# Optimization experiments

Measured on AMD Instinct MI355X. Metric: run time of the kernel, lower is better.

## Reference

```python
import jax, jax.numpy as jnp
import numpy as np

B, S, D, H = 2, 2048, 1024, 16
DK = D // H
NEG = -1.0e9


def setup_inputs() -> dict:
    key = jax.random.key(0)
    ks = jax.random.split(key, 11)
    inp = {
        "q": jax.random.normal(ks[0], (B, S, D), jnp.float32),
        "k": jax.random.normal(ks[1], (B, S, D), jnp.float32),
        "v": jax.random.normal(ks[2], (B, S, D), jnp.float32),
        "mask": jnp.tril(jnp.ones((S, S), jnp.int32))[None, None],  # causal [1,1,S,S]
    }
    scale = 0.02
    inp["w_q"] = jax.random.normal(ks[3], (D, D), jnp.float32) * scale
    inp["b_q"] = jnp.zeros((D,), jnp.float32)
    inp["w_k"] = jax.random.normal(ks[4], (D, D), jnp.float32) * scale
    inp["b_k"] = jnp.zeros((D,), jnp.float32)
    inp["w_v"] = jax.random.normal(ks[5], (D, D), jnp.float32) * scale
    inp["b_v"] = jnp.zeros((D,), jnp.float32)
    inp["w_o"] = jax.random.normal(ks[6], (D, D), jnp.float32) * scale
    inp["b_o"] = jnp.zeros((D,), jnp.float32)
    return inp


def reference(q, k, v, mask, w_q, b_q, w_k, b_k, w_v, b_v, w_o, b_o):
    # projections: [B,S,D] -> [B,H,S,DK]
    def proj(x, w, b):
        y = jnp.einsum("bsd,de->bse", x, w) + b
        return y.reshape(B, S, H, DK).transpose(0, 2, 1, 3)

    Q = proj(q, w_q, b_q)
    K = proj(k, w_k, b_k)
    V = proj(v, w_v, b_v)
    # explicit scores matrix, faithful to the original naive attention
    scores = jnp.einsum("bhsd,bhtd->bhst", Q, K) / jnp.sqrt(jnp.float32(DK))
    scores = jnp.where(mask == 0, NEG, scores)
    attn = jax.nn.softmax(scores, axis=-1)  # dropout p=0.0 -> identity
    x = jnp.einsum("bhst,bhtd->bhsd", attn, V)
    x = x.transpose(0, 2, 1, 3).reshape(B, S, D)
    return jnp.einsum("bsd,de->bse", x, w_o) + b_o
```

## Files before the change

### kernel.cpp

```cpp
#include <hip/hip_runtime.h>
#include <hip/hip_bf16.h>

typedef __bf16 bf16;
typedef __bf16 bf16x2 __attribute__((ext_vector_type(2)));
typedef __bf16 bf16x8 __attribute__((ext_vector_type(8)));
typedef float f32x4 __attribute__((ext_vector_type(4)));
typedef float f32x16 __attribute__((ext_vector_type(16)));

#define MFMA16(a, b, c) __builtin_amdgcn_mfma_f32_16x16x32_bf16(a, b, c, 0, 0, 0)
#define MFMA32(a, b, c) __builtin_amdgcn_mfma_f32_32x32x16_bf16(a, b, c, 0, 0, 0)

#define QSCALE 0.18033688f

__device__ __forceinline__ void gld16(const bf16* g, bf16* l) {
  __builtin_amdgcn_global_load_lds(
      (const __attribute__((address_space(1))) void*)g,
      (__attribute__((address_space(3))) void*)l, 16, 0, 0);
}

__global__ __launch_bounds__(256) void prep_k(
    const float* __restrict__ w0, const float* __restrict__ w1,
    const float* __restrict__ w2, const float* __restrict__ w3,
    bf16* __restrict__ dst, const float* __restrict__ q,
    const float* __restrict__ k, const float* __restrict__ v,
    bf16* __restrict__ qb, bf16* __restrict__ kb, bf16* __restrict__ vb) {
  const int t = threadIdx.x;
  if (blockIdx.z >= 4) {
    const int zi = blockIdx.z - 4;
    const float* src = zi == 0 ? q : zi == 1 ? k : v;
    bf16* d = zi == 0 ? qb : zi == 1 ? kb : vb;
    const int fb = blockIdx.y * 16 + blockIdx.x;
#pragma unroll
    for (int j = 0; j < 8; ++j) {
      const size_t i = ((size_t)j * 65536 + fb * 256 + t) * 8;
      float4 a = *(const float4*)(src + i);
      float4 b = *(const float4*)(src + i + 4);
      bf16x8 o;
      o[0] = (bf16)a.x; o[1] = (bf16)a.y; o[2] = (bf16)a.z; o[3] = (bf16)a.w;
      o[4] = (bf16)b.x; o[5] = (bf16)b.y; o[6] = (bf16)b.z; o[7] = (bf16)b.w;
      *(bf16x8*)(d + i) = o;
    }
    return;
  }

  __shared__ bf16 T[64][68];
  const float* W = blockIdx.z == 0 ? w0 : blockIdx.z == 1 ? w1
                   : blockIdx.z == 2 ? w2 : w3;
  bf16* Y = dst + (size_t)blockIdx.z * 1024 * 1024;
  const int r = t >> 2, c4 = t & 3;
  const int k0 = blockIdx.y * 64, n0 = blockIdx.x * 64;

  const float4* src = (const float4*)(W + (size_t)(k0 + r) * 1024 + n0 + c4 * 16);
  float4 f0 = src[0], f1 = src[1], f2 = src[2], f3 = src[3];
  bf16* row = &T[r][c4 * 16];
  row[0] = (bf16)f0.x; row[1] = (bf16)f0.y; row[2] = (bf16)f0.z; row[3] = (bf16)f0.w;
  row[4] = (bf16)f1.x; row[5] = (bf16)f1.y; row[6] = (bf16)f1.z; row[7] = (bf16)f1.w;
  row[8] = (bf16)f2.x; row[9] = (bf16)f2.y; row[10] = (bf16)f2.z; row[11] = (bf16)f2.w;
  row[12] = (bf16)f3.x; row[13] = (bf16)f3.y; row[14] = (bf16)f3.z; row[15] = (bf16)f3.w;
  __syncthreads();

  bf16x8 o0, o1;
#pragma unroll
  for (int j = 0; j < 8; ++j) o0[j] = T[c4 * 16 + j][r];
#pragma unroll
  for (int j = 0; j < 8; ++j) o1[j] = T[c4 * 16 + 8 + j][r];
  bf16* d = Y + (size_t)(n0 + r) * 1024 + k0 + c4 * 16;
  *(bf16x8*)d = o0;
  *(bf16x8*)(d + 8) = o1;
}

template <int QKV, int MT>
__global__ __launch_bounds__(256, 3) void gemm_p(
    const bf16* __restrict__ xq, const bf16* __restrict__ xk,
    const bf16* __restrict__ xv, const bf16* __restrict__ Wt,
    const float* __restrict__ bq, const float* __restrict__ bk,
    const float* __restrict__ bv, bf16* __restrict__ Qp,
    bf16* __restrict__ Kp, bf16* __restrict__ Vtp, float* __restrict__ Yf) {
  constexpr int AROWS = MT * 32;
  __shared__ __align__(16) bf16 SH[AROWS * 64 + 128 * 64];
  bf16* Al = SH;
  bf16* Bl = SH + AROWS * 64;

  const int z = QKV ? blockIdx.z : 0;
  const bf16* X = QKV ? (z == 0 ? xq : z == 1 ? xk : xv) : xq;
  const bf16* Bt = Wt + (size_t)z * 1048576;
  const float* bias = QKV ? (z == 0 ? bq : z == 1 ? bk : bv) : bq;
  const float escale = (QKV && z == 0) ? QSCALE : 1.0f;

  const int t = threadIdx.x;
  const int wave = t >> 6, lane = t & 63, quad = lane >> 4, l16 = lane & 15;
  const int wm = (wave >> 1) * (MT * 16), wn = (wave & 1) * 64;
  const int bm = blockIdx.y * AROWS, bn = blockIdx.x * 128;

  const int lr = (lane >> 3) & 7, lc = lane & 7;
  constexpr int NAC = AROWS / 32;
  const bf16* gA[NAC];
  bf16* lA[NAC];
#pragma unroll
  for (int i = 0; i < NAC; ++i) {
    const int q = wave * NAC + i;
    gA[i] = X + (size_t)(bm + 8 * q + lr) * 1024 + 8 * (lc ^ lr);
    lA[i] = Al + q * 512;
  }
  const bf16* gB[4];
  bf16* lB[4];
#pragma unroll
  for (int i = 0; i < 4; ++i) {
    const int q = wave * 4 + i;
    gB[i] = Bt + (size_t)(bn + 8 * q + lr) * 1024 + 8 * (lc ^ lr);
    lB[i] = Bl + q * 512;
  }

  f32x4 acc[MT][4] = {};
  const int fswz = (l16 & 7) << 4;

  for (int kb = 0; kb < 1024; kb += 64) {
    __syncthreads();
#pragma unroll
    for (int i = 0; i < NAC; ++i) gld16(gA[i] + kb, lA[i]);
#pragma unroll
    for (int i = 0; i < 4; ++i) gld16(gB[i] + kb, lB[i]);
    __syncthreads();

#pragma unroll
    for (int kk = 0; kk < 2; ++kk) {
      const int cb = (kk * 64 + quad * 16) ^ fswz;
      bf16x8 af[MT], bfr[4];
#pragma unroll
      for (int mt = 0; mt < MT; ++mt)
        af[mt] = *(const bf16x8*)((const char*)Al +
                                  (wm + mt * 16 + l16) * 128 + cb);
#pragma unroll
      for (int nt = 0; nt < 4; ++nt)
        bfr[nt] = *(const bf16x8*)((const char*)Bl +
                                   (wn + nt * 16 + l16) * 128 + cb);
#pragma unroll
      for (int mt = 0; mt < MT; ++mt)
#pragma unroll
        for (int nt = 0; nt < 4; ++nt)
          acc[mt][nt] = MFMA16(af[mt], bfr[nt], acc[mt][nt]);
    }
  }

  if (QKV && z == 2) {
    bf16* Tt = SH;
    const int b = bm >> 11;
    __syncthreads();
#pragma unroll
    for (int half = 0; half < 2; ++half) {
      if ((wave & 1) == half) {
#pragma unroll
        for (int nt = 0; nt < 4; ++nt) {
          const int ln = nt * 16 + l16;
          const float bia = bias[bn + half * 64 + ln];
#pragma unroll
          for (int mt = 0; mt < 4; ++mt)
#pragma unroll
            for (int r = 0; r < 4; ++r) {
              const int m = wm + mt * 16 + quad * 4 + r;
              Tt[ln * 136 + m] = (bf16)(acc[mt][nt][r] + bia);
            }
        }
      }
      __syncthreads();
      {
        const int ln = t >> 2, seg = (t & 3) * 32;
        const int gn = bn + half * 64 + ln;
        const int h = gn >> 6, dk = gn & 63;
        const int s0 = (bm & 2047) + seg;
        bf16* dstp = Vtp + ((size_t)(b * 16 + h) * 64 + dk) * 2048 + s0;
        const bf16* srcp = Tt + ln * 136 + seg;
#pragma unroll
        for (int j = 0; j < 4; ++j)
          *(bf16x8*)(dstp + j * 8) = *(const bf16x8*)(srcp + j * 8);
      }
      __syncthreads();
    }
  } else {
#pragma unroll
    for (int mt = 0; mt < MT; ++mt)
#pragma unroll
      for (int nt = 0; nt < 4; ++nt) {
        const int gn = bn + wn + nt * 16 + l16;
        const float bia = bias[gn];
#pragma unroll
        for (int r = 0; r < 4; ++r) {
          const int gm = bm + wm + mt * 16 + quad * 4 + r;
          const float val = (acc[mt][nt][r] + bia) * escale;
          if (!QKV) {
            Yf[(size_t)gm * 1024 + gn] = val;
          } else {
            const int b = gm >> 11, s = gm & 2047;
            const int h = gn >> 6, dk = gn & 63;
            bf16* Y = (z == 0) ? Qp : Kp;
            Y[((size_t)(b * 16 + h) * 2048 + s) * 64 + dk] = (bf16)val;
          }
        }
      }
  }
}

__global__ __launch_bounds__(256, 2) void attn_k(const bf16* __restrict__ Q,
                                                 const bf16* __restrict__ K,
                                                 const bf16* __restrict__ Vt,
                                                 bf16* __restrict__ X) {
  __shared__ __align__(16) char LB[65536];
  __shared__ float Ex[2048];
  __shared__ float ExR[128];
  __shared__ float rsL[4][32];

  bf16* KB = (bf16*)LB;
  bf16* VB = (bf16*)(LB + 32768);

  const int t = threadIdx.x;
  const int wave = t >> 6, lane = t & 63;
  const int cl = lane & 31, h = lane >> 5;
  const int qsub = wave & 1, kpart = wave >> 1;

  const int n = blockIdx.x;
  const int xcd = n & 7, mm = n >> 3;
  const int bh = xcd + 8 * (mm & 3);
  const int pairx = mm >> 2;
  const int b = bh >> 4, hh = bh & 15;

  const bf16* Qb = Q + (size_t)bh * 2048 * 64;
  const bf16* Kb = K + (size_t)bh * 2048 * 64;
  const bf16* Vb = Vt + (size_t)bh * 64 * 2048;

  const int lr = (lane >> 3) & 7, lc = lane & 7;
  const int sp = wave & 1;
  const bool isV = wave >= 2;
  const bf16* gsb = isV ? (Vb + (size_t)lr * 2048 + 8 * (lc ^ lr))
                        : (Kb + (size_t)lr * 64 + 8 * (lc ^ lr));
  const size_t cqStep = isV ? 16384 : 512;
  const size_t ktStep = isV ? 64 : 4096;
  bf16* lbs = (isV ? VB : KB) + sp * 4096;

  const int fswz = (cl & 7) << 4;

  for (int ph = 0; ph < 2; ++ph) {
    const int qt = ph ? 31 - pairx : pairx;
    const int ntiles = qt + 1;
    const int S = (ntiles + 1) >> 1;
    const int q0 = qt * 64 + qsub * 32;

    bf16x8 qf[4];
#pragma unroll
    for (int ks = 0; ks < 4; ++ks)
      qf[ks] = *(const bf16x8*)(Qb + (size_t)(q0 + cl) * 64 + ks * 16 + h * 8);

    f32x16 o0 = {}, o1 = {};
    float rs = 0.f;

#pragma unroll
    for (int cq = 0; cq < 8; ++cq)
      gld16(gsb + (size_t)sp * ktStep + cq * cqStep, lbs + cq * 512);
    __syncthreads();

    for (int ss = 0; ss < S; ++ss) {
      const int par = ss & 1;
      const bool more = (ss + 1) < S;
      if (more) {
        const size_t kt2 = 2 * (ss + 1) + sp;
#pragma unroll
        for (int cq = 0; cq < 8; ++cq)
          gld16(gsb + kt2 * ktStep + cq * cqStep,
                lbs + (par ^ 1) * 8192 + cq * 512);
      }

      const int kt = 2 * ss + kpart;
      if (kt < ntiles) {
        const int k0 = kt * 64;
        const char* Kc = (const char*)(KB + (par * 2 + kpart) * 4096);
        const char* Vc = (const char*)(VB + (par * 2 + kpart) * 4096);
        const bool interior = (k0 + 63) <= q0;

        f32x16 s0v = {}, s1v = {};
#pragma unroll
        for (int ks = 0; ks < 4; ++ks) {
          const int cb = ks * 32 + h * 16;
          bf16x8 f0 = *(const bf16x8*)(Kc + cl * 128 + (cb ^ fswz));
          bf16x8 f1 = *(const bf16x8*)(Kc + (cl + 32) * 128 + (cb ^ fswz));
          s0v = MFMA32(f0, qf[ks], s0v);
          s1v = MFMA32(f1, qf[ks], s1v);
        }

        unsigned pk[8][2];
        float ts = 0.f;
        auto smax = [&](const f32x16& sv, int mk) {
#pragma unroll
          for (int sl = 0; sl < 4; ++sl)
#pragma unroll
            for (int p = 0; p < 2; ++p) {
              float e0 = exp2f(sv[sl * 4 + 2 * p]);
              float e1 = exp2f(sv[sl * 4 + 2 * p + 1]);
              if (!interior) {
                const int ky = k0 + mk * 32 + 8 * sl + 4 * h + 2 * p;
                const int qg = q0 + cl;
                if (ky > qg) e0 = 0.f;
                if (ky + 1 > qg) e1 = 0.f;
              }
              ts += e0 + e1;
              union { bf16x2 v; unsigned u; } cv;
              cv.v[0] = (bf16)e0;
              cv.v[1] = (bf16)e1;
              pk[mk * 4 + sl][p] = cv.u;
            }
        };
        smax(s0v, 0);
        smax(s1v, 1);
        rs += ts;

        bf16x8 pf[4];
#pragma unroll
        for (int ks = 0; ks < 4; ++ks) {
          const unsigned oe0 = pk[2 * ks][0], oe1 = pk[2 * ks][1];
          const unsigned oo0 = pk[2 * ks + 1][0], oo1 = pk[2 * ks + 1][1];
          const unsigned pe0 = (unsigned)__shfl_xor((int)oe0, 32, 64);
          const unsigned pe1 = (unsigned)__shfl_xor((int)oe1, 32, 64);
          const unsigned po0 = (unsigned)__shfl_xor((int)oo0, 32, 64);
          const unsigned po1 = (unsigned)__shfl_xor((int)oo1, 32, 64);
          union { unsigned u[4]; bf16x8 v; } fu;
          fu.u[0] = h ? po0 : oe0;
          fu.u[1] = h ? po1 : oe1;
          fu.u[2] = h ? oo0 : pe0;
          fu.u[3] = h ? oo1 : pe1;
          pf[ks] = fu.v;
        }

#pragma unroll
        for (int ks = 0; ks < 4; ++ks) {
          const int cb = ks * 32 + h * 16;
          bf16x8 v0f = *(const bf16x8*)(Vc + cl * 128 + (cb ^ fswz));
          bf16x8 v1f = *(const bf16x8*)(Vc + (cl + 32) * 128 + (cb ^ fswz));
          o0 = MFMA32(pf[ks], v0f, o0);
          o1 = MFMA32(pf[ks], v1f, o1);
        }
      }

      __syncthreads();
    }

    if (kpart == 0) {
      float* e = Ex + qsub * 1024;
#pragma unroll
      for (int i = 0; i < 16; ++i) e[i * 64 + lane] = o0[i];
      ExR[qsub * 64 + lane] = rs;
    }
    __syncthreads();
    if (kpart == 1) {
      const float* e = Ex + qsub * 1024;
#pragma unroll
      for (int i = 0; i < 16; ++i) o0[i] += e[i * 64 + lane];
      rs += ExR[qsub * 64 + lane];
    }
    __syncthreads();
    if (kpart == 0) {
      float* e = Ex + qsub * 1024;
#pragma unroll
      for (int i = 0; i < 16; ++i) e[i * 64 + lane] = o1[i];
    }
    __syncthreads();
    if (kpart == 1) {
      const float* e = Ex + qsub * 1024;
#pragma unroll
      for (int i = 0; i < 16; ++i) o1[i] += e[i * 64 + lane];

      const float rtot = rs + __shfl_xor(rs, 32, 64);
      rsL[wave][cl] = 1.0f / rtot;
      __builtin_amdgcn_s_waitcnt(0xC07F);
      bf16* Xb = X + (size_t)b * 2048 * 1024 + hh * 64;
#pragma unroll
      for (int g = 0; g < 16; ++g) {
        const int qr = (g & 3) + 8 * (g >> 2) + 4 * h;
        const float ri = rsL[wave][qr];
        const int qg = q0 + qr;
        Xb[(size_t)qg * 1024 + cl] = (bf16)(o0[g] * ri);
        Xb[(size_t)qg * 1024 + 32 + cl] = (bf16)(o1[g] * ri);
      }
    }
    __syncthreads();
  }
}

extern "C" void kernel_launch(void* const* d_in, const int* in_sizes, int n_in,
                              void* d_out, int out_size, void* d_ws,
                              size_t ws_size, hipStream_t stream) {
  const float* q = (const float*)d_in[0];
  const float* k = (const float*)d_in[1];
  const float* v = (const float*)d_in[2];
  const float* w_q = (const float*)d_in[4];
  const float* b_q = (const float*)d_in[5];
  const float* w_k = (const float*)d_in[6];
  const float* b_k = (const float*)d_in[7];
  const float* w_v = (const float*)d_in[8];
  const float* b_v = (const float*)d_in[9];
  const float* w_o = (const float*)d_in[10];
  const float* b_o = (const float*)d_in[11];

  bf16* ws = (bf16*)d_ws;
  const size_t NELEM = (size_t)4096 * 1024;
  bf16* Qp = ws;
  bf16* Kp = ws + NELEM;
  bf16* Vtp = ws + 2 * NELEM;
  bf16* Xp = ws + 3 * NELEM;
  bf16* Wt = ws + 4 * NELEM;
  bf16* Wto = Wt + 3145728;
  bf16* qb = Xp;
  bf16* kb = (bf16*)d_out;
  bf16* vb = kb + NELEM;

  prep_k<<<dim3(16, 16, 7), 256, 0, stream>>>(w_q, w_k, w_v, w_o, Wt, q, k, v,
                                              qb, kb, vb);

  gemm_p<1, 4><<<dim3(8, 32, 3), 256, 0, stream>>>(
      qb, kb, vb, Wt, b_q, b_k, b_v, Qp, Kp, Vtp, nullptr);
  attn_k<<<dim3(512), 256, 0, stream>>>(Qp, Kp, Vtp, Xp);
  gemm_p<0, 2><<<dim3(8, 64), 256, 0, stream>>>(
      Xp, nullptr, nullptr, Wto, b_o, nullptr, nullptr, nullptr, nullptr,
      nullptr, (float*)d_out);
}
```

Before: 230.7 us.

## Drop LDS K/V staging, load fragments from global, split keys across four waves

The attention kernel no longer stages K and V tiles into shared memory with async global-to-LDS loads and per-step barriers. Each wave now reads its K and V MFMA fragments straight from global memory and processes every fourth key tile. The block grows to 512 threads so each 32-row query half has four key partitions, and partial outputs and row sums are reduced through shared memory at the end. This removes the per-tile barriers and LDS traffic but adds redundant global/L2 reads and uncoalesced fragment loads, and the reduction now combines four partitions instead of two.

```diff
diff --git a/kernel.cpp b/kernel.cpp
--- a/kernel.cpp
+++ b/kernel.cpp
@@ -200,22 +200,18 @@
   }
 }
 
-__global__ __launch_bounds__(256, 2) void attn_k(const bf16* __restrict__ Q,
+__global__ __launch_bounds__(512, 4) void attn_k(const bf16* __restrict__ Q,
                                                  const bf16* __restrict__ K,
                                                  const bf16* __restrict__ Vt,
                                                  bf16* __restrict__ X) {
-  __shared__ __align__(16) char LB[65536];
-  __shared__ float Ex[2048];
-  __shared__ float ExR[128];
-  __shared__ float rsL[4][32];
-
-  bf16* KB = (bf16*)LB;
-  bf16* VB = (bf16*)(LB + 32768);
+  __shared__ float Ex[3][2][1024];
+  __shared__ float ExR[3][2][64];
+  __shared__ float rsL[2][32];
 
   const int t = threadIdx.x;
   const int wave = t >> 6, lane = t & 63;
   const int cl = lane & 31, h = lane >> 5;
-  const int qsub = wave & 1, kpart = wave >> 1;
+  const int qsub = wave & 1, kp = wave >> 1;
 
   const int n = blockIdx.x;
   const int xcd = n & 7, mm = n >> 3;
@@ -227,21 +223,9 @@
   const bf16* Kb = K + (size_t)bh * 2048 * 64;
   const bf16* Vb = Vt + (size_t)bh * 64 * 2048;
 
-  const int lr = (lane >> 3) & 7, lc = lane & 7;
-  const int sp = wave & 1;
-  const bool isV = wave >= 2;
-  const bf16* gsb = isV ? (Vb + (size_t)lr * 2048 + 8 * (lc ^ lr))
-                        : (Kb + (size_t)lr * 64 + 8 * (lc ^ lr));
-  const size_t cqStep = isV ? 16384 : 512;
-  const size_t ktStep = isV ? 64 : 4096;
-  bf16* lbs = (isV ? VB : KB) + sp * 4096;
-
-  const int fswz = (cl & 7) << 4;
-
   for (int ph = 0; ph < 2; ++ph) {
     const int qt = ph ? 31 - pairx : pairx;
     const int ntiles = qt + 1;
-    const int S = (ntiles + 1) >> 1;
     const int q0 = qt * 64 + qsub * 32;
 
     bf16x8 qf[4];
@@ -252,128 +236,123 @@
     f32x16 o0 = {}, o1 = {};
     float rs = 0.f;
 
-#pragma unroll
-    for (int cq = 0; cq < 8; ++cq)
-      gld16(gsb + (size_t)sp * ktStep + cq * cqStep, lbs + cq * 512);
-    __syncthreads();
-
-    for (int ss = 0; ss < S; ++ss) {
-      const int par = ss & 1;
-      const bool more = (ss + 1) < S;
-      if (more) {
-        const size_t kt2 = 2 * (ss + 1) + sp;
-#pragma unroll
-        for (int cq = 0; cq < 8; ++cq)
-          gld16(gsb + kt2 * ktStep + cq * cqStep,
-                lbs + (par ^ 1) * 8192 + cq * 512);
-      }
-
-      const int kt = 2 * ss + kpart;
-      if (kt < ntiles) {
-        const int k0 = kt * 64;
-        const char* Kc = (const char*)(KB + (par * 2 + kpart) * 4096);
-        const char* Vc = (const char*)(VB + (par * 2 + kpart) * 4096);
-        const bool interior = (k0 + 63) <= q0;
-
-        f32x16 s0v = {}, s1v = {};
-#pragma unroll
-        for (int ks = 0; ks < 4; ++ks) {
-          const int cb = ks * 32 + h * 16;
-          bf16x8 f0 = *(const bf16x8*)(Kc + cl * 128 + (cb ^ fswz));
-          bf16x8 f1 = *(const bf16x8*)(Kc + (cl + 32) * 128 + (cb ^ fswz));
-          s0v = MFMA32(f0, qf[ks], s0v);
-          s1v = MFMA32(f1, qf[ks], s1v);
-        }
-
-        unsigned pk[8][2];
-        float ts = 0.f;
-        auto smax = [&](const f32x16& sv, int mk) {
-#pragma unroll
-          for (int sl = 0; sl < 4; ++sl)
-#pragma unroll
-            for (int p = 0; p < 2; ++p) {
-              float e0 = exp2f(sv[sl * 4 + 2 * p]);
-              float e1 = exp2f(sv[sl * 4 + 2 * p + 1]);
-              if (!interior) {
-                const int ky = k0 + mk * 32 + 8 * sl + 4 * h + 2 * p;
-                const int qg = q0 + cl;
-                if (ky > qg) e0 = 0.f;
-                if (ky + 1 > qg) e1 = 0.f;
-              }
-              ts += e0 + e1;
-              union { bf16x2 v; unsigned u; } cv;
-              cv.v[0] = (bf16)e0;
-              cv.v[1] = (bf16)e1;
-              pk[mk * 4 + sl][p] = cv.u;
+    for (int kt = kp; kt < ntiles; kt += 4) {
+      const int k0 = kt * 64;
+      const bool interior = (k0 + 63) <= q0;
+
+      const bf16* Kt0 = Kb + (size_t)(k0 + cl) * 64 + h * 8;
+      const bf16* Kt1 = Kb + (size_t)(k0 + cl + 32) * 64 + h * 8;
+      bf16x8 kf0[4], kf1[4];
+#pragma unroll
+      for (int ks = 0; ks < 4; ++ks) {
+        kf0[ks] = *(const bf16x8*)(Kt0 + ks * 16);
+        kf1[ks] = *(const bf16x8*)(Kt1 + ks * 16);
+      }
+      f32x16 s0v = {}, s1v = {};
+#pragma unroll
+      for (int ks = 0; ks < 4; ++ks) {
+        s0v = MFMA32(kf0[ks], qf[ks], s0v);
+        s1v = MFMA32(kf1[ks], qf[ks], s1v);
+      }
+
+      const bf16* Vr0 = Vb + (size_t)cl * 2048 + k0 + h * 8;
+      const bf16* Vr1 = Vb + (size_t)(cl + 32) * 2048 + k0 + h * 8;
+      bf16x8 vf0[4], vf1[4];
+#pragma unroll
+      for (int ks = 0; ks < 4; ++ks) {
+        vf0[ks] = *(const bf16x8*)(Vr0 + ks * 16);
+        vf1[ks] = *(const bf16x8*)(Vr1 + ks * 16);
+      }
+
+      unsigned pk[8][2];
+      float ts = 0.f;
+      auto smax = [&](const f32x16& sv, int mk) {
+#pragma unroll
+        for (int sl = 0; sl < 4; ++sl)
+#pragma unroll
+          for (int p = 0; p < 2; ++p) {
+            float e0 = exp2f(sv[sl * 4 + 2 * p]);
+            float e1 = exp2f(sv[sl * 4 + 2 * p + 1]);
+            if (!interior) {
+              const int ky = k0 + mk * 32 + 8 * sl + 4 * h + 2 * p;
+              const int qg = q0 + cl;
+              if (ky > qg) e0 = 0.f;
+              if (ky + 1 > qg) e1 = 0.f;
             }
-        };
-        smax(s0v, 0);
-        smax(s1v, 1);
-        rs += ts;
-
-        bf16x8 pf[4];
-#pragma unroll
-        for (int ks = 0; ks < 4; ++ks) {
-          const unsigned oe0 = pk[2 * ks][0], oe1 = pk[2 * ks][1];
-          const unsigned oo0 = pk[2 * ks + 1][0], oo1 = pk[2 * ks + 1][1];
-          const unsigned pe0 = (unsigned)__shfl_xor((int)oe0, 32, 64);
-          const unsigned pe1 = (unsigned)__shfl_xor((int)oe1, 32, 64);
-          const unsigned po0 = (unsigned)__shfl_xor((int)oo0, 32, 64);
-          const unsigned po1 = (unsigned)__shfl_xor((int)oo1, 32, 64);
-          union { unsigned u[4]; bf16x8 v; } fu;
-          fu.u[0] = h ? po0 : oe0;
-          fu.u[1] = h ? po1 : oe1;
-          fu.u[2] = h ? oo0 : pe0;
-          fu.u[3] = h ? oo1 : pe1;
-          pf[ks] = fu.v;
-        }
-
-#pragma unroll
-        for (int ks = 0; ks < 4; ++ks) {
-          const int cb = ks * 32 + h * 16;
-          bf16x8 v0f = *(const bf16x8*)(Vc + cl * 128 + (cb ^ fswz));
-          bf16x8 v1f = *(const bf16x8*)(Vc + (cl + 32) * 128 + (cb ^ fswz));
-          o0 = MFMA32(pf[ks], v0f, o0);
-          o1 = MFMA32(pf[ks], v1f, o1);
-        }
-      }
-
-      __syncthreads();
-    }
-
-    if (kpart == 0) {
-      float* e = Ex + qsub * 1024;
+            ts += e0 + e1;
+            union { bf16x2 v; unsigned u; } cv;
+            cv.v[0] = (bf16)e0;
+            cv.v[1] = (bf16)e1;
+            pk[mk * 4 + sl][p] = cv.u;
+          }
+      };
+      smax(s0v, 0);
+      smax(s1v, 1);
+      rs += ts;
+
+      bf16x8 pf[4];
+#pragma unroll
+      for (int ks = 0; ks < 4; ++ks) {
+        const unsigned oe0 = pk[2 * ks][0], oe1 = pk[2 * ks][1];
+        const unsigned oo0 = pk[2 * ks + 1][0], oo1 = pk[2 * ks + 1][1];
+        const unsigned pe0 = (unsigned)__shfl_xor((int)oe0, 32, 64);
+        const unsigned pe1 = (unsigned)__shfl_xor((int)oe1, 32, 64);
+        const unsigned po0 = (unsigned)__shfl_xor((int)oo0, 32, 64);
+        const unsigned po1 = (unsigned)__shfl_xor((int)oo1, 32, 64);
+        union { unsigned u[4]; bf16x8 v; } fu;
+        fu.u[0] = h ? po0 : oe0;
+        fu.u[1] = h ? po1 : oe1;
+        fu.u[2] = h ? oo0 : pe0;
+        fu.u[3] = h ? oo1 : pe1;
+        pf[ks] = fu.v;
+      }
+
+#pragma unroll
+      for (int ks = 0; ks < 4; ++ks) {
+        o0 = MFMA32(pf[ks], vf0[ks], o0);
+        o1 = MFMA32(pf[ks], vf1[ks], o1);
+      }
+    }
+
+    if (kp > 0) {
+      float* e = &Ex[kp - 1][qsub][0];
 #pragma unroll
       for (int i = 0; i < 16; ++i) e[i * 64 + lane] = o0[i];
-      ExR[qsub * 64 + lane] = rs;
-    }
-    __syncthreads();
-    if (kpart == 1) {
-      const float* e = Ex + qsub * 1024;
-#pragma unroll
-      for (int i = 0; i < 16; ++i) o0[i] += e[i * 64 + lane];
-      rs += ExR[qsub * 64 + lane];
-    }
-    __syncthreads();
-    if (kpart == 0) {
-      float* e = Ex + qsub * 1024;
+      ExR[kp - 1][qsub][lane] = rs;
+    }
+    __syncthreads();
+    if (kp == 0) {
+#pragma unroll
+      for (int w = 0; w < 3; ++w) {
+        const float* e = &Ex[w][qsub][0];
+#pragma unroll
+        for (int i = 0; i < 16; ++i) o0[i] += e[i * 64 + lane];
+        rs += ExR[w][qsub][lane];
+      }
+    }
+    __syncthreads();
+    if (kp > 0) {
+      float* e = &Ex[kp - 1][qsub][0];
 #pragma unroll
       for (int i = 0; i < 16; ++i) e[i * 64 + lane] = o1[i];
     }
     __syncthreads();
-    if (kpart == 1) {
-      const float* e = Ex + qsub * 1024;
-#pragma unroll
-      for (int i = 0; i < 16; ++i) o1[i] += e[i * 64 + lane];
+    if (kp == 0) {
+#pragma unroll
+      for (int w = 0; w < 3; ++w) {
+        const float* e = &Ex[w][qsub][0];
+#pragma unroll
+        for (int i = 0; i < 16; ++i) o1[i] += e[i * 64 + lane];
+      }
 
       const float rtot = rs + __shfl_xor(rs, 32, 64);
-      rsL[wave][cl] = 1.0f / rtot;
+      rsL[qsub][cl] = 1.0f / rtot;
       __builtin_amdgcn_s_waitcnt(0xC07F);
       bf16* Xb = X + (size_t)b * 2048 * 1024 + hh * 64;
 #pragma unroll
       for (int g = 0; g < 16; ++g) {
         const int qr = (g & 3) + 8 * (g >> 2) + 4 * h;
-        const float ri = rsL[wave][qr];
+        const float ri = rsL[qsub][qr];
         const int qg = q0 + qr;
         Xb[(size_t)qg * 1024 + cl] = (bf16)(o0[g] * ri);
         Xb[(size_t)qg * 1024 + 32 + cl] = (bf16)(o1[g] * ri);
@@ -415,7 +394,7 @@
 
   gemm_p<1, 4><<<dim3(8, 32, 3), 256, 0, stream>>>(
       qb, kb, vb, Wt, b_q, b_k, b_v, Qp, Kp, Vtp, nullptr);
-  attn_k<<<dim3(512), 256, 0, stream>>>(Qp, Kp, Vtp, Xp);
+  attn_k<<<dim3(512), 512, 0, stream>>>(Qp, Kp, Vtp, Xp);
   gemm_p<0, 2><<<dim3(8, 64), 256, 0, stream>>>(
       Xp, nullptr, nullptr, Wto, b_o, nullptr, nullptr, nullptr, nullptr,
       nullptr, (float*)d_out);
```

New measurement: 265.1 us. 14.9% more time.
